# Optimization experiments

Hardware: AMD Instinct MI355X
Metric: run time of the kernel (lower is better)

Reference implementation:

```python
import jax, jax.numpy as jnp
import numpy as np

D_MODEL = 384
HEAD_SIZE = 64
B, T = 64, 512


def setup_inputs() -> dict:
    key = jax.random.key(0)
    kx, kq, kk, kv = jax.random.split(key, 4)
    x = jax.random.normal(kx, (B, T, D_MODEL), dtype=jnp.float32)
    Wq = jax.random.normal(kq, (D_MODEL, HEAD_SIZE), dtype=jnp.float32) * 0.02
    Wk = jax.random.normal(kk, (D_MODEL, HEAD_SIZE), dtype=jnp.float32) * 0.02
    Wv = jax.random.normal(kv, (D_MODEL, HEAD_SIZE), dtype=jnp.float32) * 0.02
    return {"x": x, "Wq": Wq, "Wk": Wk, "Wv": Wv}


def reference(x, Wq, Wk, Wv):
    # x: [B, T, C]; projections (bias-free linear layers)
    q = jnp.einsum("btc,ch->bth", x, Wq)  # [B, T, H]
    k = jnp.einsum("btc,ch->bth", x, Wk)
    v = jnp.einsum("btc,ch->bth", x, Wv)
    Tn = x.shape[1]
    scale = 1.0 / jnp.sqrt(jnp.float32(k.shape[-1]))
    wei = jnp.einsum("bqh,bkh->bqk", q, k) * scale  # [B, T, T]
    causal = jnp.tril(jnp.ones((Tn, Tn), dtype=bool))
    wei = jnp.where(causal, wei, -jnp.inf)
    wei = jax.nn.softmax(wei, axis=-1)
    # dropout omitted (eval mode) for deterministic reference
    out = jnp.einsum("bqk,bkh->bqh", wei, v)  # [B, T, H]
    return out
```

## Files before the change

### kernel.cpp

```cpp
#include <hip/hip_runtime.h>
#include <math.h>

#define NB 64
#define NT 512
#define NC 384
#define NH 64

typedef __attribute__((ext_vector_type(8))) short bf16x8;
typedef __attribute__((ext_vector_type(4))) float f32x4;

__device__ __forceinline__ unsigned short f2bf(float f) {
  unsigned int u = __float_as_uint(f);
  return (unsigned short)((u + 0x7FFFu + ((u >> 16) & 1u)) >> 16);
}
__device__ __forceinline__ unsigned int pk2bf(float a, float b) {
  return (unsigned int)f2bf(a) | ((unsigned int)f2bf(b) << 16);
}
__device__ __forceinline__ bf16x8 pack8(float4 lo, float4 hi) {
  union { bf16x8 v; unsigned short s[8]; } u;
  u.s[0] = f2bf(lo.x); u.s[1] = f2bf(lo.y); u.s[2] = f2bf(lo.z); u.s[3] = f2bf(lo.w);
  u.s[4] = f2bf(hi.x); u.s[5] = f2bf(hi.y); u.s[6] = f2bf(hi.z); u.s[7] = f2bf(hi.w);
  return u.v;
}

__global__ __launch_bounds__(256) void wtrans_kernel(
    const float* __restrict__ Wq, const float* __restrict__ Wk,
    const float* __restrict__ Wv, unsigned short* __restrict__ Wt) {
  int id = blockIdx.x * 256 + threadIdx.x;
  if (id >= 3 * NC * NH) return;
  int m = id / (NC * NH);
  int r = id % (NC * NH);
  int c = r / NH;
  int h = r % NH;
  const float* W = (m == 0) ? Wq : ((m == 1) ? Wk : Wv);
  Wt[(m * NH + h) * NC + c] = f2bf(W[c * NH + h]);
}

#define WSTR 136
__global__ __launch_bounds__(256) void proj_kernel(
    const float* __restrict__ x, const unsigned short* __restrict__ Wt,
    unsigned short* __restrict__ q, unsigned short* __restrict__ k,
    unsigned short* __restrict__ vt) {
  __shared__ unsigned short ws[192 * WSTR];
  const int t = threadIdx.x;
  const int m0 = blockIdx.x * 64;
  const int w = t >> 6, l = t & 63, mi = l & 15, quad = l >> 4;

  f32x4 acc[12];
  const f32x4 zero = {0.f, 0.f, 0.f, 0.f};
#pragma unroll
  for (int i = 0; i < 12; ++i) acc[i] = zero;

  const float* xrow = x + (size_t)(m0 + w * 16 + mi) * NC;

  for (int ko = 0; ko < 3; ++ko) {
    if (ko) __syncthreads();
#pragma unroll
    for (int i = 0; i < 12; ++i) {
      int u = t + i * 256;
      int row = u >> 4, seg = u & 15;
      *(uint4*)&ws[row * WSTR + seg * 8] =
          *(const uint4*)&Wt[row * NC + ko * 128 + seg * 8];
    }
    __syncthreads();
#pragma unroll
    for (int kci = 0; kci < 4; ++kci) {
      const float* xp = xrow + ko * 128 + kci * 32 + quad * 8;
      float4 lo = *(const float4*)xp;
      float4 hi = *(const float4*)(xp + 4);
      bf16x8 a = pack8(lo, hi);
#pragma unroll
      for (int nt = 0; nt < 12; ++nt) {
        bf16x8 bf = *(const bf16x8*)&ws[(nt * 16 + mi) * WSTR + kci * 32 + quad * 8];
        acc[nt] = __builtin_amdgcn_mfma_f32_16x16x32_bf16(a, bf, acc[nt], 0, 0, 0);
      }
    }
  }

  const int rbase = m0 + w * 16 + quad * 4;
#pragma unroll
  for (int nt = 0; nt < 4; ++nt)
#pragma unroll
    for (int r = 0; r < 4; ++r)
      q[(size_t)(rbase + r) * NH + nt * 16 + mi] = f2bf(acc[nt][r] * 0.125f);
#pragma unroll
  for (int nt = 4; nt < 8; ++nt)
#pragma unroll
    for (int r = 0; r < 4; ++r)
      k[(size_t)(rbase + r) * NH + (nt - 4) * 16 + mi] = f2bf(acc[nt][r]);

  __syncthreads();
#pragma unroll
  for (int nt = 8; nt < 12; ++nt) {
    int h = (nt - 8) * 16 + mi;
#pragma unroll
    for (int r = 0; r < 4; ++r)
      ws[h * 72 + w * 16 + quad * 4 + r] = f2bf(acc[nt][r]);
  }
  __syncthreads();
  {
    int bb = m0 >> 9, t0 = m0 & 511;
#pragma unroll
    for (int i = 0; i < 2; ++i) {
      int u = t + i * 256;
      int h = u >> 3, seg = u & 7;
      *(uint4*)&vt[((size_t)bb * NH + h) * NT + t0 + seg * 8] =
          *(const uint4*)&ws[h * 72 + seg * 8];
    }
  }
}

#define PSTR 72
__global__ __launch_bounds__(64) void attn_kernel(
    const unsigned short* __restrict__ q, const unsigned short* __restrict__ k,
    const unsigned short* __restrict__ vt, float* __restrict__ out) {
  __shared__ unsigned short ps[16 * PSTR];
  const int l = threadIdx.x;
  const int mi = l & 15, quad = l >> 4;
  const int bx = blockIdx.x;
  const int qi = 31 - (bx >> 6);
  const int b = bx & 63;

  const unsigned short* qrow = q + ((size_t)b * NT + qi * 16 + mi) * NH;
  bf16x8 qb0 = *(const bf16x8*)(qrow + quad * 8);
  bf16x8 qb1 = *(const bf16x8*)(qrow + 32 + quad * 8);

  f32x4 accO[4];
  const f32x4 zero = {0.f, 0.f, 0.f, 0.f};
#pragma unroll
  for (int i = 0; i < 4; ++i) accO[i] = zero;
  float mrow = -INFINITY, lrow = 0.f;

  const int ktmax = (qi * 16 + 15) >> 6;
  for (int kt = 0; kt <= ktmax; ++kt) {
    const unsigned short* kb = k + ((size_t)b * NT + kt * 64) * NH;
    const unsigned short* vb = vt + (size_t)b * NH * NT + kt * 64;
    bf16x8 ka0[4], ka1[4], va0[4], va1[4];
#pragma unroll
    for (int nt = 0; nt < 4; ++nt) {
      const unsigned short* kr = kb + (size_t)(nt * 16 + mi) * NH + quad * 8;
      ka0[nt] = *(const bf16x8*)kr;
      ka1[nt] = *(const bf16x8*)(kr + 32);
      const unsigned short* vr = vb + (size_t)(nt * 16 + mi) * NT + quad * 8;
      va0[nt] = *(const bf16x8*)vr;
      va1[nt] = *(const bf16x8*)(vr + 32);
    }

    float p[4][4];
#pragma unroll
    for (int nt = 0; nt < 4; ++nt) {
      f32x4 z = zero;
      z = __builtin_amdgcn_mfma_f32_16x16x32_bf16(ka0[nt], qb0, z, 0, 0, 0);
      z = __builtin_amdgcn_mfma_f32_16x16x32_bf16(ka1[nt], qb1, z, 0, 0, 0);
#pragma unroll
      for (int r = 0; r < 4; ++r) p[nt][r] = z[r];
    }

    if (kt == ktmax) {
#pragma unroll
      for (int nt = 0; nt < 4; ++nt)
#pragma unroll
        for (int r = 0; r < 4; ++r)
          if (kt * 64 + nt * 16 + quad * 4 + r > qi * 16 + mi)
            p[nt][r] = -INFINITY;
    }

    float vmax = -INFINITY;
#pragma unroll
    for (int nt = 0; nt < 4; ++nt)
#pragma unroll
      for (int r = 0; r < 4; ++r) vmax = fmaxf(vmax, p[nt][r]);
    vmax = fmaxf(vmax, __shfl_xor(vmax, 16));
    vmax = fmaxf(vmax, __shfl_xor(vmax, 32));
    float mn = fmaxf(mrow, vmax);
    float alpha = __expf(mrow - mn);
    mrow = mn;

    float rsum = 0.f;
#pragma unroll
    for (int nt = 0; nt < 4; ++nt)
#pragma unroll
      for (int r = 0; r < 4; ++r) {
        p[nt][r] = __expf(p[nt][r] - mn);
        rsum += p[nt][r];
      }
    rsum += __shfl_xor(rsum, 16);
    rsum += __shfl_xor(rsum, 32);
    lrow = lrow * alpha + rsum;

#pragma unroll
    for (int nt = 0; nt < 4; ++nt) {
      uint2 pk;
      pk.x = pk2bf(p[nt][0], p[nt][1]);
      pk.y = pk2bf(p[nt][2], p[nt][3]);
      *(uint2*)&ps[mi * PSTR + nt * 16 + quad * 4] = pk;
    }
    bf16x8 pa0 = *(const bf16x8*)&ps[mi * PSTR + quad * 8];
    bf16x8 pa1 = *(const bf16x8*)&ps[mi * PSTR + 32 + quad * 8];

    float av[4];
#pragma unroll
    for (int r = 0; r < 4; ++r) av[r] = __shfl(alpha, quad * 4 + r);
#pragma unroll
    for (int hi = 0; hi < 4; ++hi)
#pragma unroll
      for (int r = 0; r < 4; ++r) accO[hi][r] *= av[r];

#pragma unroll
    for (int hi = 0; hi < 4; ++hi) {
      accO[hi] = __builtin_amdgcn_mfma_f32_16x16x32_bf16(pa0, va0[hi], accO[hi], 0, 0, 0);
      accO[hi] = __builtin_amdgcn_mfma_f32_16x16x32_bf16(pa1, va1[hi], accO[hi], 0, 0, 0);
    }
  }

  float inv = 1.f / lrow;
  const size_t obase = ((size_t)b * NT + qi * 16) * NH;
#pragma unroll
  for (int r = 0; r < 4; ++r) {
    float iv = __shfl(inv, quad * 4 + r);
#pragma unroll
    for (int hi = 0; hi < 4; ++hi)
      out[obase + (size_t)(quad * 4 + r) * NH + hi * 16 + mi] = accO[hi][r] * iv;
  }
}

extern "C" void kernel_launch(void* const* d_in, const int* in_sizes, int n_in,
                              void* d_out, int out_size, void* d_ws, size_t ws_size,
                              hipStream_t stream) {
  const float* x  = (const float*)d_in[0];
  const float* Wq = (const float*)d_in[1];
  const float* Wk = (const float*)d_in[2];
  const float* Wv = (const float*)d_in[3];

  unsigned short* Wt = (unsigned short*)d_ws;
  unsigned short* qb = Wt + 192 * 384;
  unsigned short* kb = qb + 32768 * 64;
  unsigned short* vtb = kb + 32768 * 64;
  float* out = (float*)d_out;

  wtrans_kernel<<<288, 256, 0, stream>>>(Wq, Wk, Wv, Wt);
  proj_kernel<<<512, 256, 0, stream>>>(x, Wt, qb, kb, vtb);
  attn_kernel<<<2048, 64, 0, stream>>>(qb, kb, vtb, out);
}
```

Measured before the change: 128.0 us.

## Double-buffer K/V loads in attention and stage bf16 x in LDS for projection

The attention kernel now prefetches the next 64-key K/V tile into a second register set while the current tile is processed, hiding global load latency behind MFMA and softmax work. The projection kernel converts each 64-row x block to bf16 into LDS once and streams weight fragments straight from global/L2 into registers with a two-stage prefetch, instead of staging weights through LDS in three synchronized chunks. This raises register pressure in both kernels, which may lower occupancy.

New measurement: 147.4 us. 1.15x slower.

```diff
diff --git a/kernel.cpp b/kernel.cpp
--- a/kernel.cpp
+++ b/kernel.cpp
@@ -15,12 +15,6 @@
 }
 __device__ __forceinline__ unsigned int pk2bf(float a, float b) {
   return (unsigned int)f2bf(a) | ((unsigned int)f2bf(b) << 16);
-}
-__device__ __forceinline__ bf16x8 pack8(float4 lo, float4 hi) {
-  union { bf16x8 v; unsigned short s[8]; } u;
-  u.s[0] = f2bf(lo.x); u.s[1] = f2bf(lo.y); u.s[2] = f2bf(lo.z); u.s[3] = f2bf(lo.w);
-  u.s[4] = f2bf(hi.x); u.s[5] = f2bf(hi.y); u.s[6] = f2bf(hi.z); u.s[7] = f2bf(hi.w);
-  return u.v;
 }
 
 __global__ __launch_bounds__(256) void wtrans_kernel(
@@ -36,45 +30,60 @@
   Wt[(m * NH + h) * NC + c] = f2bf(W[c * NH + h]);
 }
 
-#define WSTR 136
+#define XS 392
 __global__ __launch_bounds__(256) void proj_kernel(
     const float* __restrict__ x, const unsigned short* __restrict__ Wt,
     unsigned short* __restrict__ q, unsigned short* __restrict__ k,
     unsigned short* __restrict__ vt) {
-  __shared__ unsigned short ws[192 * WSTR];
+  __shared__ unsigned short xs[64 * XS];
   const int t = threadIdx.x;
   const int m0 = blockIdx.x * 64;
   const int w = t >> 6, l = t & 63, mi = l & 15, quad = l >> 4;
 
+  const unsigned short* wp = Wt + (size_t)mi * NC + quad * 8;
+
+  bf16x8 b0[12], b1[12];
+#pragma unroll
+  for (int nt = 0; nt < 12; ++nt)
+    b0[nt] = *(const bf16x8*)(wp + (size_t)nt * 16 * NC);
+
+  for (int i = 0; i < 24; ++i) {
+    int u = t + i * 256;
+    int row = u / 96;
+    int cp = (u % 96) * 4;
+    float4 a = *(const float4*)(x + (size_t)(m0 + row) * NC + cp);
+    ushort4 bb;
+    bb.x = f2bf(a.x); bb.y = f2bf(a.y); bb.z = f2bf(a.z); bb.w = f2bf(a.w);
+    *(ushort4*)&xs[row * XS + cp] = bb;
+  }
+  __syncthreads();
+
   f32x4 acc[12];
   const f32x4 zero = {0.f, 0.f, 0.f, 0.f};
 #pragma unroll
   for (int i = 0; i < 12; ++i) acc[i] = zero;
 
-  const float* xrow = x + (size_t)(m0 + w * 16 + mi) * NC;
-
-  for (int ko = 0; ko < 3; ++ko) {
-    if (ko) __syncthreads();
-#pragma unroll
-    for (int i = 0; i < 12; ++i) {
-      int u = t + i * 256;
-      int row = u >> 4, seg = u & 15;
-      *(uint4*)&ws[row * WSTR + seg * 8] =
-          *(const uint4*)&Wt[row * NC + ko * 128 + seg * 8];
+  const unsigned short* arow = &xs[(w * 16 + mi) * XS + quad * 8];
+
+#pragma unroll
+  for (int kc2 = 0; kc2 < 6; ++kc2) {
+    const int kcA = kc2 * 2, kcB = kc2 * 2 + 1;
+#pragma unroll
+    for (int nt = 0; nt < 12; ++nt)
+      b1[nt] = *(const bf16x8*)(wp + (size_t)nt * 16 * NC + kcB * 32);
+    bf16x8 a = *(const bf16x8*)(arow + kcA * 32);
+#pragma unroll
+    for (int nt = 0; nt < 12; ++nt)
+      acc[nt] = __builtin_amdgcn_mfma_f32_16x16x32_bf16(a, b0[nt], acc[nt], 0, 0, 0);
+    if (kc2 < 5) {
+#pragma unroll
+      for (int nt = 0; nt < 12; ++nt)
+        b0[nt] = *(const bf16x8*)(wp + (size_t)nt * 16 * NC + (kcA + 2) * 32);
     }
-    __syncthreads();
-#pragma unroll
-    for (int kci = 0; kci < 4; ++kci) {
-      const float* xp = xrow + ko * 128 + kci * 32 + quad * 8;
-      float4 lo = *(const float4*)xp;
-      float4 hi = *(const float4*)(xp + 4);
-      bf16x8 a = pack8(lo, hi);
-#pragma unroll
-      for (int nt = 0; nt < 12; ++nt) {
-        bf16x8 bf = *(const bf16x8*)&ws[(nt * 16 + mi) * WSTR + kci * 32 + quad * 8];
-        acc[nt] = __builtin_amdgcn_mfma_f32_16x16x32_bf16(a, bf, acc[nt], 0, 0, 0);
-      }
-    }
+    a = *(const bf16x8*)(arow + kcB * 32);
+#pragma unroll
+    for (int nt = 0; nt < 12; ++nt)
+      acc[nt] = __builtin_amdgcn_mfma_f32_16x16x32_bf16(a, b1[nt], acc[nt], 0, 0, 0);
   }
 
   const int rbase = m0 + w * 16 + quad * 4;
@@ -95,7 +104,7 @@
     int h = (nt - 8) * 16 + mi;
 #pragma unroll
     for (int r = 0; r < 4; ++r)
-      ws[h * 72 + w * 16 + quad * 4 + r] = f2bf(acc[nt][r]);
+      xs[h * 72 + w * 16 + quad * 4 + r] = f2bf(acc[nt][r]);
   }
   __syncthreads();
   {
@@ -105,12 +114,80 @@
       int u = t + i * 256;
       int h = u >> 3, seg = u & 7;
       *(uint4*)&vt[((size_t)bb * NH + h) * NT + t0 + seg * 8] =
-          *(const uint4*)&ws[h * 72 + seg * 8];
+          *(const uint4*)&xs[h * 72 + seg * 8];
     }
   }
 }
 
 #define PSTR 72
+
+#define LOADKV(KA0, KA1, VA0, VA1, kt_)                                   \
+  do {                                                                    \
+    const unsigned short* kb_ = k + ((size_t)b * NT + (kt_) * 64) * NH;   \
+    const unsigned short* vb_ = vt + (size_t)b * NH * NT + (kt_) * 64;    \
+    _Pragma("unroll") for (int nt = 0; nt < 4; ++nt) {                    \
+      const unsigned short* kr = kb_ + (size_t)(nt * 16 + mi) * NH + quad * 8; \
+      KA0[nt] = *(const bf16x8*)kr;                                       \
+      KA1[nt] = *(const bf16x8*)(kr + 32);                                \
+      const unsigned short* vr = vb_ + (size_t)(nt * 16 + mi) * NT + quad * 8; \
+      VA0[nt] = *(const bf16x8*)vr;                                       \
+      VA1[nt] = *(const bf16x8*)(vr + 32);                                \
+    }                                                                     \
+  } while (0)
+
+#define PROCESS(KA0, KA1, VA0, VA1, kt_)                                  \
+  do {                                                                    \
+    float p[4][4];                                                        \
+    _Pragma("unroll") for (int nt = 0; nt < 4; ++nt) {                    \
+      f32x4 z = zero;                                                     \
+      z = __builtin_amdgcn_mfma_f32_16x16x32_bf16(KA0[nt], qb0, z, 0, 0, 0); \
+      z = __builtin_amdgcn_mfma_f32_16x16x32_bf16(KA1[nt], qb1, z, 0, 0, 0); \
+      _Pragma("unroll") for (int r = 0; r < 4; ++r) p[nt][r] = z[r];      \
+    }                                                                     \
+    if ((kt_) == ktmax) {                                                 \
+      _Pragma("unroll") for (int nt = 0; nt < 4; ++nt)                    \
+        _Pragma("unroll") for (int r = 0; r < 4; ++r)                     \
+          if ((kt_) * 64 + nt * 16 + quad * 4 + r > qi * 16 + mi)         \
+            p[nt][r] = -INFINITY;                                         \
+    }                                                                     \
+    float vmax = -INFINITY;                                               \
+    _Pragma("unroll") for (int nt = 0; nt < 4; ++nt)                      \
+      _Pragma("unroll") for (int r = 0; r < 4; ++r)                       \
+        vmax = fmaxf(vmax, p[nt][r]);                                     \
+    vmax = fmaxf(vmax, __shfl_xor(vmax, 16));                             \
+    vmax = fmaxf(vmax, __shfl_xor(vmax, 32));                             \
+    float mn = fmaxf(mrow, vmax);                                         \
+    float alpha = __expf(mrow - mn);                                      \
+    mrow = mn;                                                            \
+    float rsum = 0.f;                                                     \
+    _Pragma("unroll") for (int nt = 0; nt < 4; ++nt)                      \
+      _Pragma("unroll") for (int r = 0; r < 4; ++r) {                     \
+        p[nt][r] = __expf(p[nt][r] - mn);                                 \
+        rsum += p[nt][r];                                                 \
+      }                                                                   \
+    rsum += __shfl_xor(rsum, 16);                                         \
+    rsum += __shfl_xor(rsum, 32);                                         \
+    lrow = lrow * alpha + rsum;                                           \
+    _Pragma("unroll") for (int nt = 0; nt < 4; ++nt) {                    \
+      uint2 pk;                                                           \
+      pk.x = pk2bf(p[nt][0], p[nt][1]);                                   \
+      pk.y = pk2bf(p[nt][2], p[nt][3]);                                   \
+      *(uint2*)&ps[mi * PSTR + nt * 16 + quad * 4] = pk;                  \
+    }                                                                     \
+    bf16x8 pa0 = *(const bf16x8*)&ps[mi * PSTR + quad * 8];               \
+    bf16x8 pa1 = *(const bf16x8*)&ps[mi * PSTR + 32 + quad * 8];          \
+    float av[4];                                                          \
+    _Pragma("unroll") for (int r = 0; r < 4; ++r)                         \
+      av[r] = __shfl(alpha, quad * 4 + r);                                \
+    _Pragma("unroll") for (int hi = 0; hi < 4; ++hi)                      \
+      _Pragma("unroll") for (int r = 0; r < 4; ++r)                       \
+        accO[hi][r] *= av[r];                                             \
+    _Pragma("unroll") for (int hi = 0; hi < 4; ++hi) {                    \
+      accO[hi] = __builtin_amdgcn_mfma_f32_16x16x32_bf16(pa0, VA0[hi], accO[hi], 0, 0, 0); \
+      accO[hi] = __builtin_amdgcn_mfma_f32_16x16x32_bf16(pa1, VA1[hi], accO[hi], 0, 0, 0); \
+    }                                                                     \
+  } while (0)
+
 __global__ __launch_bounds__(64) void attn_kernel(
     const unsigned short* __restrict__ q, const unsigned short* __restrict__ k,
     const unsigned short* __restrict__ vt, float* __restrict__ out) {
@@ -132,85 +209,19 @@
   float mrow = -INFINITY, lrow = 0.f;
 
   const int ktmax = (qi * 16 + 15) >> 6;
-  for (int kt = 0; kt <= ktmax; ++kt) {
-    const unsigned short* kb = k + ((size_t)b * NT + kt * 64) * NH;
-    const unsigned short* vb = vt + (size_t)b * NH * NT + kt * 64;
-    bf16x8 ka0[4], ka1[4], va0[4], va1[4];
-#pragma unroll
-    for (int nt = 0; nt < 4; ++nt) {
-      const unsigned short* kr = kb + (size_t)(nt * 16 + mi) * NH + quad * 8;
-      ka0[nt] = *(const bf16x8*)kr;
-      ka1[nt] = *(const bf16x8*)(kr + 32);
-      const unsigned short* vr = vb + (size_t)(nt * 16 + mi) * NT + quad * 8;
-      va0[nt] = *(const bf16x8*)vr;
-      va1[nt] = *(const bf16x8*)(vr + 32);
-    }
-
-    float p[4][4];
-#pragma unroll
-    for (int nt = 0; nt < 4; ++nt) {
-      f32x4 z = zero;
-      z = __builtin_amdgcn_mfma_f32_16x16x32_bf16(ka0[nt], qb0, z, 0, 0, 0);
-      z = __builtin_amdgcn_mfma_f32_16x16x32_bf16(ka1[nt], qb1, z, 0, 0, 0);
-#pragma unroll
-      for (int r = 0; r < 4; ++r) p[nt][r] = z[r];
-    }
-
-    if (kt == ktmax) {
-#pragma unroll
-      for (int nt = 0; nt < 4; ++nt)
-#pragma unroll
-        for (int r = 0; r < 4; ++r)
-          if (kt * 64 + nt * 16 + quad * 4 + r > qi * 16 + mi)
-            p[nt][r] = -INFINITY;
-    }
-
-    float vmax = -INFINITY;
-#pragma unroll
-    for (int nt = 0; nt < 4; ++nt)
-#pragma unroll
-      for (int r = 0; r < 4; ++r) vmax = fmaxf(vmax, p[nt][r]);
-    vmax = fmaxf(vmax, __shfl_xor(vmax, 16));
-    vmax = fmaxf(vmax, __shfl_xor(vmax, 32));
-    float mn = fmaxf(mrow, vmax);
-    float alpha = __expf(mrow - mn);
-    mrow = mn;
-
-    float rsum = 0.f;
-#pragma unroll
-    for (int nt = 0; nt < 4; ++nt)
-#pragma unroll
-      for (int r = 0; r < 4; ++r) {
-        p[nt][r] = __expf(p[nt][r] - mn);
-        rsum += p[nt][r];
-      }
-    rsum += __shfl_xor(rsum, 16);
-    rsum += __shfl_xor(rsum, 32);
-    lrow = lrow * alpha + rsum;
-
-#pragma unroll
-    for (int nt = 0; nt < 4; ++nt) {
-      uint2 pk;
-      pk.x = pk2bf(p[nt][0], p[nt][1]);
-      pk.y = pk2bf(p[nt][2], p[nt][3]);
-      *(uint2*)&ps[mi * PSTR + nt * 16 + quad * 4] = pk;
-    }
-    bf16x8 pa0 = *(const bf16x8*)&ps[mi * PSTR + quad * 8];
-    bf16x8 pa1 = *(const bf16x8*)&ps[mi * PSTR + 32 + quad * 8];
-
-    float av[4];
-#pragma unroll
-    for (int r = 0; r < 4; ++r) av[r] = __shfl(alpha, quad * 4 + r);
-#pragma unroll
-    for (int hi = 0; hi < 4; ++hi)
-#pragma unroll
-      for (int r = 0; r < 4; ++r) accO[hi][r] *= av[r];
-
-#pragma unroll
-    for (int hi = 0; hi < 4; ++hi) {
-      accO[hi] = __builtin_amdgcn_mfma_f32_16x16x32_bf16(pa0, va0[hi], accO[hi], 0, 0, 0);
-      accO[hi] = __builtin_amdgcn_mfma_f32_16x16x32_bf16(pa1, va1[hi], accO[hi], 0, 0, 0);
-    }
+
+  bf16x8 k0a[4], k0b[4], v0a[4], v0b[4];
+  bf16x8 k1a[4], k1b[4], v1a[4], v1b[4];
+  LOADKV(k0a, k0b, v0a, v0b, 0);
+
+  int kt = 0;
+  while (true) {
+    if (kt + 1 <= ktmax) LOADKV(k1a, k1b, v1a, v1b, kt + 1);
+    PROCESS(k0a, k0b, v0a, v0b, kt);
+    if (++kt > ktmax) break;
+    if (kt + 1 <= ktmax) LOADKV(k0a, k0b, v0a, v0b, kt + 1);
+    PROCESS(k1a, k1b, v1a, v1b, kt);
+    if (++kt > ktmax) break;
   }
 
   float inv = 1.f / lrow;
```

## Restructure projection kernel: stage x in LDS, keep weight fragments in registers

Applied to the files above, without the earlier changes.

The projection kernel now uses 6 waves per block. Each wave owns two of the twelve output column tiles and holds the bf16 weight fragments for those tiles in registers. The x tile is converted to bf16 once and staged in LDS, so the weights no longer stream through LDS in three chunks with repeated barriers. The V transpose store is written directly from registers as ushort4 chunks instead of going through an LDS transpose. This costs a large register footprint (24 bf16x8 fragments plus accumulators) under launch_bounds(384,3), and the vt stores are narrower and less coalesced.

After: 121.9 us. 1.05x faster.

```diff
diff --git a/kernel.cpp b/kernel.cpp
--- a/kernel.cpp
+++ b/kernel.cpp
@@ -15,12 +15,6 @@
 }
 __device__ __forceinline__ unsigned int pk2bf(float a, float b) {
   return (unsigned int)f2bf(a) | ((unsigned int)f2bf(b) << 16);
-}
-__device__ __forceinline__ bf16x8 pack8(float4 lo, float4 hi) {
-  union { bf16x8 v; unsigned short s[8]; } u;
-  u.s[0] = f2bf(lo.x); u.s[1] = f2bf(lo.y); u.s[2] = f2bf(lo.z); u.s[3] = f2bf(lo.w);
-  u.s[4] = f2bf(hi.x); u.s[5] = f2bf(hi.y); u.s[6] = f2bf(hi.z); u.s[7] = f2bf(hi.w);
-  return u.v;
 }
 
 __global__ __launch_bounds__(256) void wtrans_kernel(
@@ -36,76 +30,86 @@
   Wt[(m * NH + h) * NC + c] = f2bf(W[c * NH + h]);
 }
 
-#define WSTR 136
-__global__ __launch_bounds__(256) void proj_kernel(
+#define XS 392
+__global__ __launch_bounds__(384, 3) void proj_kernel(
     const float* __restrict__ x, const unsigned short* __restrict__ Wt,
     unsigned short* __restrict__ q, unsigned short* __restrict__ k,
     unsigned short* __restrict__ vt) {
-  __shared__ unsigned short ws[192 * WSTR];
+  __shared__ unsigned short xs[64 * XS];
   const int t = threadIdx.x;
   const int m0 = blockIdx.x * 64;
-  const int w = t >> 6, l = t & 63, mi = l & 15, quad = l >> 4;
-
-  f32x4 acc[12];
+  const int w = t / 64, l = t & 63, mi = l & 15, quad = l >> 4;
+
+#pragma unroll 4
+  for (int i = 0; i < 16; ++i) {
+    int u = t + i * 384;
+    int row = u / 96;
+    int cp = (u % 96) * 4;
+    float4 a = *(const float4*)(x + (size_t)(m0 + row) * NC + cp);
+    ushort4 bb;
+    bb.x = f2bf(a.x); bb.y = f2bf(a.y); bb.z = f2bf(a.z); bb.w = f2bf(a.w);
+    *(ushort4*)&xs[row * XS + cp] = bb;
+  }
+
+  bf16x8 bfr[2][12];
+#pragma unroll
+  for (int ntl = 0; ntl < 2; ++ntl) {
+    const unsigned short* wr =
+        Wt + (size_t)((w * 2 + ntl) * 16 + mi) * NC + quad * 8;
+#pragma unroll
+    for (int kc = 0; kc < 12; ++kc)
+      bfr[ntl][kc] = *(const bf16x8*)(wr + kc * 32);
+  }
+  __syncthreads();
+
+  f32x4 acc[2][4];
   const f32x4 zero = {0.f, 0.f, 0.f, 0.f};
 #pragma unroll
-  for (int i = 0; i < 12; ++i) acc[i] = zero;
-
-  const float* xrow = x + (size_t)(m0 + w * 16 + mi) * NC;
-
-  for (int ko = 0; ko < 3; ++ko) {
-    if (ko) __syncthreads();
-#pragma unroll
-    for (int i = 0; i < 12; ++i) {
-      int u = t + i * 256;
-      int row = u >> 4, seg = u & 15;
-      *(uint4*)&ws[row * WSTR + seg * 8] =
-          *(const uint4*)&Wt[row * NC + ko * 128 + seg * 8];
-    }
-    __syncthreads();
-#pragma unroll
-    for (int kci = 0; kci < 4; ++kci) {
-      const float* xp = xrow + ko * 128 + kci * 32 + quad * 8;
-      float4 lo = *(const float4*)xp;
-      float4 hi = *(const float4*)(xp + 4);
-      bf16x8 a = pack8(lo, hi);
-#pragma unroll
-      for (int nt = 0; nt < 12; ++nt) {
-        bf16x8 bf = *(const bf16x8*)&ws[(nt * 16 + mi) * WSTR + kci * 32 + quad * 8];
-        acc[nt] = __builtin_amdgcn_mfma_f32_16x16x32_bf16(a, bf, acc[nt], 0, 0, 0);
+  for (int i = 0; i < 2; ++i)
+#pragma unroll
+    for (int j = 0; j < 4; ++j) acc[i][j] = zero;
+
+#pragma unroll
+  for (int msub = 0; msub < 4; ++msub) {
+#pragma unroll
+    for (int kc = 0; kc < 12; ++kc) {
+      bf16x8 a = *(const bf16x8*)&xs[(msub * 16 + mi) * XS + kc * 32 + quad * 8];
+      acc[0][msub] =
+          __builtin_amdgcn_mfma_f32_16x16x32_bf16(a, bfr[0][kc], acc[0][msub], 0, 0, 0);
+      acc[1][msub] =
+          __builtin_amdgcn_mfma_f32_16x16x32_bf16(a, bfr[1][kc], acc[1][msub], 0, 0, 0);
+    }
+  }
+
+  if (w < 4) {
+    unsigned short* dst = (w < 2) ? q : k;
+    const float sc = (w < 2) ? 0.125f : 1.0f;
+#pragma unroll
+    for (int ntl = 0; ntl < 2; ++ntl) {
+      int tile = w * 2 + ntl;
+      int h = (tile & 3) * 16 + mi;
+#pragma unroll
+      for (int msub = 0; msub < 4; ++msub)
+#pragma unroll
+        for (int r = 0; r < 4; ++r)
+          dst[(size_t)(m0 + msub * 16 + quad * 4 + r) * NH + h] =
+              f2bf(acc[ntl][msub][r] * sc);
+    }
+  } else {
+    int bb = m0 >> 9, t0 = m0 & 511;
+#pragma unroll
+    for (int ntl = 0; ntl < 2; ++ntl) {
+      int tile = w * 2 + ntl;
+      int h = (tile & 3) * 16 + mi;
+#pragma unroll
+      for (int msub = 0; msub < 4; ++msub) {
+        ushort4 s;
+        s.x = f2bf(acc[ntl][msub][0]);
+        s.y = f2bf(acc[ntl][msub][1]);
+        s.z = f2bf(acc[ntl][msub][2]);
+        s.w = f2bf(acc[ntl][msub][3]);
+        *(ushort4*)&vt[((size_t)bb * NH + h) * NT + t0 + msub * 16 + quad * 4] = s;
       }
-    }
-  }
-
-  const int rbase = m0 + w * 16 + quad * 4;
-#pragma unroll
-  for (int nt = 0; nt < 4; ++nt)
-#pragma unroll
-    for (int r = 0; r < 4; ++r)
-      q[(size_t)(rbase + r) * NH + nt * 16 + mi] = f2bf(acc[nt][r] * 0.125f);
-#pragma unroll
-  for (int nt = 4; nt < 8; ++nt)
-#pragma unroll
-    for (int r = 0; r < 4; ++r)
-      k[(size_t)(rbase + r) * NH + (nt - 4) * 16 + mi] = f2bf(acc[nt][r]);
-
-  __syncthreads();
-#pragma unroll
-  for (int nt = 8; nt < 12; ++nt) {
-    int h = (nt - 8) * 16 + mi;
-#pragma unroll
-    for (int r = 0; r < 4; ++r)
-      ws[h * 72 + w * 16 + quad * 4 + r] = f2bf(acc[nt][r]);
-  }
-  __syncthreads();
-  {
-    int bb = m0 >> 9, t0 = m0 & 511;
-#pragma unroll
-    for (int i = 0; i < 2; ++i) {
-      int u = t + i * 256;
-      int h = u >> 3, seg = u & 7;
-      *(uint4*)&vt[((size_t)bb * NH + h) * NT + t0 + seg * 8] =
-          *(const uint4*)&ws[h * 72 + seg * 8];
     }
   }
 }
@@ -239,6 +243,6 @@
   float* out = (float*)d_out;
 
   wtrans_kernel<<<288, 256, 0, stream>>>(Wq, Wk, Wv, Wt);
-  proj_kernel<<<512, 256, 0, stream>>>(x, Wt, qb, kb, vtb);
+  proj_kernel<<<512, 384, 0, stream>>>(x, Wt, qb, kb, vtb);
   attn_kernel<<<2048, 64, 0, stream>>>(qb, kb, vtb, out);
 }
```
